# Performance work log

Measured on AMD Instinct MI355X. Metric: run time of the kernel, lower is better.

The kernel has to match this reference:

```python
import jax, jax.numpy as jnp
import numpy as np

N, IN, HID, HEADS, FFN = 2048, 768, 1024, 8, 2048
NH = HID // HEADS  # 128 per-head hidden


def setup_inputs() -> dict:
    key = jax.random.key(0)
    ks = jax.random.split(key, 24)
    s = 0.02
    inp = {
        "feature": jax.random.normal(ks[0], (1, N, IN), jnp.float32),
        "adj": jax.random.bernoulli(ks[1], 0.05, (1, N, N)).astype(jnp.float32),
        "gat1_W1": jax.random.normal(ks[2], (IN, HID), jnp.float32) * s,
        "gat1_a1": jax.random.normal(ks[3], (2 * NH,), jnp.float32) * s,
        "gat1_W2": jax.random.normal(ks[4], (HID, IN), jnp.float32) * s,
        "gat1_a2": jax.random.normal(ks[5], (2 * IN,), jnp.float32) * s,
        "gat2_W1": jax.random.normal(ks[6], (IN, HID), jnp.float32) * s,
        "gat2_a1": jax.random.normal(ks[7], (2 * NH,), jnp.float32) * s,
        "gat2_W2": jax.random.normal(ks[8], (HID, IN), jnp.float32) * s,
        "gat2_a2": jax.random.normal(ks[9], (2 * IN,), jnp.float32) * s,
        "Wf": jax.random.normal(ks[10], (2 * IN, IN), jnp.float32) * s,
        "bf": jnp.zeros((IN,), jnp.float32),
        "ffn_W1": jax.random.normal(ks[11], (IN, FFN), jnp.float32) * s,
        "ffn_b1": jnp.zeros((FFN,), jnp.float32),
        "ffn_W2": jax.random.normal(ks[12], (FFN, FFN), jnp.float32) * s,
        "ffn_b2": jnp.zeros((FFN,), jnp.float32),
        "ffn_W3": jax.random.normal(ks[13], (FFN, IN), jnp.float32) * s,
        "ffn_b3": jnp.zeros((IN,), jnp.float32),
        "out_W1": jax.random.normal(ks[14], (IN, FFN), jnp.float32) * s,
        "out_b1": jnp.zeros((FFN,), jnp.float32),
        "out_W2": jax.random.normal(ks[15], (FFN, IN), jnp.float32) * s,
        "out_b2": jnp.zeros((IN,), jnp.float32),
    }
    return inp


def leaky(x, slope):
    return jnp.where(x >= 0, x, slope * x)


def gat_layer(h, adjb, W, a, heads, concat):
    # h: [N, F_in]; adjb: [N, N] bool. Scores decompose since attn weight is
    # shared across heads: e_ij = leaky(a_l . g_i + a_r . g_j).
    n = h.shape[0]
    g = (h @ W).reshape(n, heads, -1)           # [N, H, F']
    f = g.shape[-1]
    gl = jnp.einsum("nhf,f->nh", g, a[:f])
    gr = jnp.einsum("nhf,f->nh", g, a[f:])
    e = leaky(gl[:, None, :] + gr[None, :, :], 0.2)   # [N, N, H]
    e = jnp.where(adjb[:, :, None], e, jnp.float32(-1e9))
    att = jax.nn.softmax(e, axis=1)             # softmax over source j
    out = jnp.einsum("ijh,jhf->ihf", att, g)    # [N, H, F']
    return out.reshape(n, -1) if concat else out.mean(axis=1)


def gat(x, adj2d, W1, a1, W2, a2):
    adjb = adj2d != 0
    x1 = jax.nn.elu(gat_layer(x, adjb, W1, a1, HEADS, True))
    return gat_layer(x1, adjb, W2, a2, 1, False)


def reference(feature, adj, gat1_W1, gat1_a1, gat1_W2, gat1_a2,
              gat2_W1, gat2_a1, gat2_W2, gat2_a2, Wf, bf,
              ffn_W1, ffn_b1, ffn_W2, ffn_b2, ffn_W3, ffn_b3,
              out_W1, out_b1, out_W2, out_b2):
    sen_adj = adj.at[:, :, -6:].set(0.0)
    sec_adj = jnp.zeros_like(adj).at[:, :, -6:].set(adj[:, :, -6:])
    x = feature[0]                               # [N, IN]
    f_sen = gat(x, sen_adj[0], gat1_W1, gat1_a1, gat1_W2, gat1_a2) + x
    f_sec = gat(x, sec_adj[0], gat2_W1, gat2_a1, gat2_W2, gat2_a2) + x
    f = jnp.concatenate([f_sec, f_sen], axis=-1)
    f = leaky(f @ Wf + bf, 0.01)                 # fusion linear + leaky
    # ffn: MLP(layers=3, keep_last=False) -> act on every layer
    f = leaky(f @ ffn_W1 + ffn_b1, 0.01)
    f = leaky(f @ ffn_W2 + ffn_b2, 0.01)
    f = leaky(f @ ffn_W3 + ffn_b3, 0.01)
    # out_ffn: MLP(layers=2)
    o = leaky(f @ out_W1 + out_b1, 0.01)
    o = leaky(o @ out_W2 + out_b2, 0.01)
    return (o + x)[None]                         # residual, [1, N, IN]
```

## Files before the change

kernel.cpp:

```cpp
#include <hip/hip_runtime.h>
#include <hip/hip_bf16.h>
#include <cmath>

#define NN 2048
#define DIN 768
#define DHID 1024
#define NHEADS 8
#define FPRIME 128
#define DFFN 2048
#define SEN_LIM 2042
#define MAXDEG 256

using short8 = __attribute__((ext_vector_type(8))) short;
using f32x4  = __attribute__((ext_vector_type(4))) float;

#if defined(__has_builtin)
#  if __has_builtin(__builtin_amdgcn_global_load_lds)
#    define HAVE_GLL 1
#  endif
#endif
#ifndef HAVE_GLL
#  define HAVE_GLL 0
#endif

__device__ inline unsigned short f2bf(float f) {
    unsigned u = __float_as_uint(f);
    unsigned r = u + 0x7FFFu + ((u >> 16) & 1u);
    return (unsigned short)(r >> 16);
}
__device__ inline float bf2f(unsigned short h) {
    return __uint_as_float(((unsigned)h) << 16);
}
__device__ inline void store_out(float* p, float v) { *p = v; }
__device__ inline void store_out(unsigned short* p, float v) { *p = f2bf(v); }

#if HAVE_GLL
__device__ inline void gll16(const unsigned short* g, unsigned short* l) {
    __builtin_amdgcn_global_load_lds(
        (const __attribute__((address_space(1))) unsigned int*)g,
        (__attribute__((address_space(3))) unsigned int*)l, 16, 0, 0);
}
#endif

__global__ __launch_bounds__(256) void build_nbrs(
    const float* __restrict__ adj,
    unsigned short* __restrict__ sen_idx, int* __restrict__ sen_cnt,
    unsigned short* __restrict__ sec_idx, int* __restrict__ sec_cnt)
{
    const int i = blockIdx.x;
    __shared__ int c_sen, c_sec;
    if (threadIdx.x == 0) { c_sen = 0; c_sec = 0; }
    __syncthreads();
    for (int j4 = threadIdx.x; j4 < NN / 4; j4 += 256) {
        float4 v = *(const float4*)&adj[(size_t)i * NN + j4 * 4];
        float vs[4] = {v.x, v.y, v.z, v.w};
        #pragma unroll
        for (int q = 0; q < 4; ++q) {
            if (vs[q] != 0.0f) {
                int j = j4 * 4 + q;
                if (j < SEN_LIM) {
                    int p = atomicAdd(&c_sen, 1);
                    if (p < MAXDEG) sen_idx[(size_t)i * MAXDEG + p] = (unsigned short)j;
                } else {
                    int p = atomicAdd(&c_sec, 1);
                    if (p < 8) sec_idx[i * 8 + p] = (unsigned short)j;
                }
            }
        }
    }
    __syncthreads();
    if (threadIdx.x == 0) { sen_cnt[i] = min(c_sen, MAXDEG); sec_cnt[i] = min(c_sec, 8); }
}

struct TPJob { const float* s; unsigned short* d; int K, N, start, trans; };
struct TPJobs { TPJob j[11]; };

__global__ __launch_bounds__(256) void mega_tp(TPJobs jobs, int njobs)
{
    __shared__ float t[32][33];
    const int tile = blockIdx.x;
    int ji = 0;
    for (int k = 1; k < 11; ++k)
        if (k < njobs && tile >= jobs.j[k].start) ji = k;
    const TPJob jb = jobs.j[ji];
    const int lt = tile - jb.start;
    const int ntx = jb.N >> 5;
    const int bn = (lt % ntx) * 32, bk = (lt / ntx) * 32;
    const int tx = threadIdx.x & 31, ty = threadIdx.x >> 5;
    if (jb.trans) {
        #pragma unroll
        for (int r = 0; r < 4; ++r)
            t[ty + r * 8][tx] = jb.s[(size_t)(bk + ty + r * 8) * jb.N + bn + tx];
        __syncthreads();
        #pragma unroll
        for (int r = 0; r < 4; ++r) {
            int n = ty + r * 8;
            jb.d[(size_t)(bn + n) * jb.K + bk + tx] = f2bf(t[tx][n]);
        }
    } else {
        #pragma unroll
        for (int r = 0; r < 4; ++r) {
            size_t e = (size_t)(bk + ty + r * 8) * jb.N + bn + tx;
            jb.d[e] = f2bf(jb.s[e]);
        }
    }
}

template<int BM, int BN, typename OUT_T>
__global__ __launch_bounds__(256) void gemm_mfma(
    const unsigned short* __restrict__ A0, const unsigned short* __restrict__ A1,
    const unsigned short* __restrict__ BT0, const unsigned short* __restrict__ BT1,
    const float* __restrict__ bias, const float* __restrict__ resid,
    OUT_T* __restrict__ C0, OUT_T* __restrict__ C1,
    unsigned short* __restrict__ Cb0, unsigned short* __restrict__ Cb1,
    int M, int N, int K, int act)
{
    constexpr int BK = 64;
    constexpr int WR = BM / 64;
    constexpr int WC = 4 / WR;
    constexpr int NF = BN / (WC * 16);
    constexpr int ACH = BM / 32;
    constexpr int BCH = BN / 32;
    __shared__ unsigned short Asm[BM * BK];
    __shared__ unsigned short Bsm[BN * BK];
    const int z = blockIdx.z;
    const unsigned short* A  = z ? A1  : A0;
    const unsigned short* BT = z ? BT1 : BT0;
    OUT_T* C = z ? C1 : C0;
    unsigned short* Cb = z ? Cb1 : Cb0;
    const int tid = threadIdx.x;
    const int lane = tid & 63, w = tid >> 6;
    const int wr = w / WC, wc = w % WC;
    const int bm = blockIdx.y * BM, bn = blockIdx.x * BN;

    f32x4 acc[4][NF];
    #pragma unroll
    for (int mi = 0; mi < 4; ++mi)
        #pragma unroll
        for (int ni = 0; ni < NF; ++ni)
            acc[mi][ni] = (f32x4){0.f, 0.f, 0.f, 0.f};

    const unsigned short* Abase = A + (size_t)bm * K;
    const unsigned short* Bbase = BT + (size_t)bn * K;

    for (int k0 = 0; k0 < K; k0 += BK) {
        __syncthreads();
        #pragma unroll
        for (int c = 0; c < ACH; ++c) {
            int e = (tid + c * 256) * 8;
            int r = e >> 6, kk = e & 63;
            int kks = kk ^ ((r & 7) << 3);
#if HAVE_GLL
            gll16(&Abase[(size_t)r * K + k0 + kks], &Asm[e]);
#else
            *(short8*)&Asm[e] = *(const short8*)&Abase[(size_t)r * K + k0 + kks];
#endif
        }
        #pragma unroll
        for (int c = 0; c < BCH; ++c) {
            int e = (tid + c * 256) * 8;
            int r = e >> 6, kk = e & 63;
            int kks = kk ^ ((r & 7) << 3);
#if HAVE_GLL
            gll16(&Bbase[(size_t)r * K + k0 + kks], &Bsm[e]);
#else
            *(short8*)&Bsm[e] = *(const short8*)&Bbase[(size_t)r * K + k0 + kks];
#endif
        }
        __syncthreads();
        #pragma unroll
        for (int ks = 0; ks < 2; ++ks) {
            short8 af[4], bfv[NF];
            #pragma unroll
            for (int mi = 0; mi < 4; ++mi) {
                int row = wr * 64 + mi * 16 + (lane & 15);
                int col = (ks * 32 + (lane >> 4) * 8) ^ ((row & 7) << 3);
                af[mi] = *(const short8*)&Asm[row * 64 + col];
            }
            #pragma unroll
            for (int ni = 0; ni < NF; ++ni) {
                int row = wc * (BN / WC) + ni * 16 + (lane & 15);
                int col = (ks * 32 + (lane >> 4) * 8) ^ ((row & 7) << 3);
                bfv[ni] = *(const short8*)&Bsm[row * 64 + col];
            }
            #pragma unroll
            for (int mi = 0; mi < 4; ++mi)
                #pragma unroll
                for (int ni = 0; ni < NF; ++ni)
                    acc[mi][ni] = __builtin_amdgcn_mfma_f32_16x16x32_bf16(
                        af[mi], bfv[ni], acc[mi][ni], 0, 0, 0);
        }
    }

    const int rbase = bm + wr * 64;
    const int cbase = bn + wc * (BN / WC);
    #pragma unroll
    for (int mi = 0; mi < 4; ++mi)
        #pragma unroll
        for (int ni = 0; ni < NF; ++ni)
            #pragma unroll
            for (int r = 0; r < 4; ++r) {
                int grow = rbase + mi * 16 + (lane >> 4) * 4 + r;
                int gcol = cbase + ni * 16 + (lane & 15);
                float v = acc[mi][ni][r];
                if (bias)  v += bias[gcol];
                if (act)   v = (v >= 0.f) ? v : 0.01f * v;
                if (resid) v += resid[(size_t)grow * N + gcol];
                store_out(&C[(size_t)grow * N + gcol], v);
                if (Cb) Cb[(size_t)grow * N + gcol] = f2bf(v);
            }
}

__global__ __launch_bounds__(64) void glgr2(
    const unsigned short* __restrict__ gA, const unsigned short* __restrict__ gB,
    int row_stride, int F, int Hlog2, int nb_per_branch,
    const float* __restrict__ aA, const float* __restrict__ aB,
    float* __restrict__ glA, float* __restrict__ grA,
    float* __restrict__ glB, float* __restrict__ grB,
    float* __restrict__ z, int zblocks)
{
    const int bid = blockIdx.x, lane = threadIdx.x;
    if (bid < zblocks) z[bid * 64 + lane] = 0.f;
    const int br = bid >= nb_per_branch;
    const int b = br ? bid - nb_per_branch : bid;
    const int node = b >> Hlog2, h = b - ((b >> Hlog2) << Hlog2);
    const unsigned short* g = (br ? gB : gA) + (size_t)node * row_stride + h * F;
    const float* a = br ? aB : aA;
    float sl = 0.f, sr = 0.f;
    for (int f = lane; f < F; f += 64) {
        float v = bf2f(g[f]);
        sl += v * a[f];
        sr += v * a[F + f];
    }
    #pragma unroll
    for (int off = 32; off > 0; off >>= 1) {
        sl += __shfl_down(sl, off);
        sr += __shfl_down(sr, off);
    }
    if (lane == 0) {
        (br ? glB : glA)[b] = sl;
        (br ? grB : grA)[b] = sr;
    }
}

__global__ __launch_bounds__(256) void col_mean2(
    const unsigned short* __restrict__ g0, const unsigned short* __restrict__ g1,
    int C, float* __restrict__ o0, float* __restrict__ o1)
{
    const unsigned short* g = blockIdx.z ? g1 : g0;
    float* o = blockIdx.z ? o1 : o0;
    int c = blockIdx.x * 256 + threadIdx.x;
    int r0 = blockIdx.y * 128;
    float s = 0.f;
    for (int r = r0; r < r0 + 128; ++r) s += bf2f(g[(size_t)r * C + c]);
    atomicAdd(&o[c], s * (1.0f / 2048.0f));
}

template<int H, int F, typename OUT_T>
__global__ __launch_bounds__(256) void attn_agg2(
    const unsigned short* __restrict__ gb0, const unsigned short* __restrict__ gb1,
    int g_stride,
    const float* __restrict__ gl0, const float* __restrict__ gr0,
    const float* __restrict__ gl1, const float* __restrict__ gr1,
    const unsigned short* __restrict__ idx0, int is0, const int* __restrict__ cnt0,
    const unsigned short* __restrict__ idx1, int is1, const int* __restrict__ cnt1,
    const float* __restrict__ gmean0, const float* __restrict__ gmean1,
    OUT_T* __restrict__ dst0, OUT_T* __restrict__ dst1,
    int dst_stride, int co0, int co1,
    const float* __restrict__ resid, int mode)
{
    constexpr int HF = H * F;
    const int bid = blockIdx.x;
    const int br = bid >= NN;
    const int i = br ? bid - NN : bid;
    const unsigned short* gbp = br ? gb1 : gb0;
    const float* gl = br ? gl1 : gl0;
    const float* gr = br ? gr1 : gr0;
    const unsigned short* idx = br ? idx1 : idx0;
    const int is = br ? is1 : is0;
    const int* cnt = br ? cnt1 : cnt0;
    const float* gmean = br ? gmean1 : gmean0;
    OUT_T* dst = br ? dst1 : dst0;
    const int co = br ? co1 : co0;

    const int tid = threadIdx.x;
    const int lane = tid & 63, w = tid >> 6;
    const int n = cnt[i];

    if (n == 0) {
        for (int c = tid; c < HF; c += 256) {
            float v = gmean[c];
            if (mode == 0) v = (v > 0.f) ? v : expm1f(v);
            else           v += resid[(size_t)i * HF + c];
            store_out(&dst[(size_t)i * dst_stride + co + c], v);
        }
        return;
    }

    __shared__ float s_wred[4 * H];
    __shared__ float s_max[H], s_inv[H], s_glh[H];
    __shared__ float s_w[128 * H];
    __shared__ unsigned short s_j[128];

    if (tid < H) s_glh[tid] = gl[(size_t)i * H + tid];
    __syncthreads();
    float glh[H];
    #pragma unroll
    for (int h = 0; h < H; ++h) glh[h] = s_glh[h];

    const unsigned short* row_idx = idx + (size_t)i * is;

    float pmax[H];
    #pragma unroll
    for (int h = 0; h < H; ++h) pmax[h] = -1e30f;
    for (int jj = tid; jj < n; jj += 256) {
        int j = row_idx[jj];
        if (H == 8) {
            float4 ga = *(const float4*)&gr[(size_t)j * 8];
            float4 gbv = *(const float4*)&gr[(size_t)j * 8 + 4];
            float sc[8] = {ga.x, ga.y, ga.z, ga.w, gbv.x, gbv.y, gbv.z, gbv.w};
            #pragma unroll
            for (int h = 0; h < H; ++h) {
                float s = glh[h] + sc[h];
                s = (s >= 0.f) ? s : 0.2f * s;
                pmax[h] = fmaxf(pmax[h], s);
            }
        } else {
            float s = glh[0] + gr[j];
            s = (s >= 0.f) ? s : 0.2f * s;
            pmax[0] = fmaxf(pmax[0], s);
        }
    }
    #pragma unroll
    for (int h = 0; h < H; ++h)
        #pragma unroll
        for (int off = 32; off > 0; off >>= 1)
            pmax[h] = fmaxf(pmax[h], __shfl_xor(pmax[h], off));
    if (lane == 0)
        #pragma unroll
        for (int h = 0; h < H; ++h) s_wred[w * H + h] = pmax[h];
    __syncthreads();
    if (tid < H)
        s_max[tid] = fmaxf(fmaxf(s_wred[tid], s_wred[H + tid]),
                           fmaxf(s_wred[2 * H + tid], s_wred[3 * H + tid]));
    __syncthreads();
    float mx[H];
    #pragma unroll
    for (int h = 0; h < H; ++h) mx[h] = s_max[h];

    float psum[H];
    #pragma unroll
    for (int h = 0; h < H; ++h) psum[h] = 0.f;
    for (int jj = tid; jj < n; jj += 256) {
        int j = row_idx[jj];
        if (H == 8) {
            float4 ga = *(const float4*)&gr[(size_t)j * 8];
            float4 gbv = *(const float4*)&gr[(size_t)j * 8 + 4];
            float sc[8] = {ga.x, ga.y, ga.z, ga.w, gbv.x, gbv.y, gbv.z, gbv.w};
            #pragma unroll
            for (int h = 0; h < H; ++h) {
                float s = glh[h] + sc[h];
                s = (s >= 0.f) ? s : 0.2f * s;
                psum[h] += expf(s - mx[h]);
            }
        } else {
            float s = glh[0] + gr[j];
            s = (s >= 0.f) ? s : 0.2f * s;
            psum[0] += expf(s - mx[0]);
        }
    }
    #pragma unroll
    for (int h = 0; h < H; ++h)
        #pragma unroll
        for (int off = 32; off > 0; off >>= 1)
            psum[h] += __shfl_xor(psum[h], off);
    if (lane == 0)
        #pragma unroll
        for (int h = 0; h < H; ++h) s_wred[w * H + h] = psum[h];
    __syncthreads();
    if (tid < H)
        s_inv[tid] = 1.f / (s_wred[tid] + s_wred[H + tid] +
                            s_wred[2 * H + tid] + s_wred[3 * H + tid]);

    const int cb = tid * 4;
    const bool active = (cb < HF);
    const int hh = (H == 8) ? (cb >> 7) : 0;
    float a0 = 0.f, a1 = 0.f, a2 = 0.f, a3 = 0.f;

    for (int c0 = 0; c0 < n; c0 += 128) {
        int m = min(128, n - c0);
        __syncthreads();
        for (int e = tid; e < m * H; e += 256) {
            int jj = (H == 8) ? (e >> 3) : e;
            int h  = (H == 8) ? (e & 7) : 0;
            int j = row_idx[c0 + jj];
            float s = glh[h] + gr[(size_t)j * H + h];
            s = (s >= 0.f) ? s : 0.2f * s;
            s_w[jj * H + h] = expf(s - s_max[h]) * s_inv[h];
            if (h == 0) s_j[jj] = (unsigned short)j;
        }
        __syncthreads();
        if (active) {
            int jj = 0;
            for (; jj + 8 <= m; jj += 8) {
                ushort4 v[8]; float wv[8];
                #pragma unroll
                for (int u = 0; u < 8; ++u) {
                    v[u] = *(const ushort4*)&gbp[(size_t)s_j[jj + u] * g_stride + cb];
                    wv[u] = s_w[(jj + u) * H + hh];
                }
                #pragma unroll
                for (int u = 0; u < 8; ++u) {
                    a0 += wv[u] * bf2f(v[u].x);
                    a1 += wv[u] * bf2f(v[u].y);
                    a2 += wv[u] * bf2f(v[u].z);
                    a3 += wv[u] * bf2f(v[u].w);
                }
            }
            for (; jj < m; ++jj) {
                ushort4 v0 = *(const ushort4*)&gbp[(size_t)s_j[jj] * g_stride + cb];
                float w0 = s_w[jj * H + hh];
                a0 += w0 * bf2f(v0.x); a1 += w0 * bf2f(v0.y);
                a2 += w0 * bf2f(v0.z); a3 += w0 * bf2f(v0.w);
            }
        }
    }

    if (active) {
        float vv[4] = {a0, a1, a2, a3};
        #pragma unroll
        for (int q = 0; q < 4; ++q) {
            float v = vv[q];
            if (mode == 0) v = (v > 0.f) ? v : expm1f(v);
            else           v += resid[(size_t)i * HF + cb + q];
            store_out(&dst[(size_t)i * dst_stride + co + cb + q], v);
        }
    }
}

extern "C" void kernel_launch(void* const* d_in, const int* in_sizes, int n_in,
                              void* d_out, int out_size, void* d_ws, size_t ws_size,
                              hipStream_t stream)
{
    const float* feature = (const float*)d_in[0];
    const float* adj     = (const float*)d_in[1];
    const float* g1W1 = (const float*)d_in[2];
    const float* g1a1 = (const float*)d_in[3];
    const float* g1W2 = (const float*)d_in[4];
    const float* g1a2 = (const float*)d_in[5];
    const float* g2W1 = (const float*)d_in[6];
    const float* g2a1 = (const float*)d_in[7];
    const float* g2W2 = (const float*)d_in[8];
    const float* g2a2 = (const float*)d_in[9];
    const float* Wf  = (const float*)d_in[10];
    const float* bfv = (const float*)d_in[11];
    const float* fW1 = (const float*)d_in[12];
    const float* fb1 = (const float*)d_in[13];
    const float* fW2 = (const float*)d_in[14];
    const float* fb2 = (const float*)d_in[15];
    const float* fW3 = (const float*)d_in[16];
    const float* fb3 = (const float*)d_in[17];
    const float* oW1 = (const float*)d_in[18];
    const float* ob1 = (const float*)d_in[19];
    const float* oW2 = (const float*)d_in[20];
    const float* ob2 = (const float*)d_in[21];
    float* out = (float*)d_out;

    char* ws = (char*)d_ws;
    size_t off = 0;
    auto alloc = [&](size_t bytes) -> void* {
        void* p = ws + off;
        off = (off + bytes + 255) & ~(size_t)255;
        return p;
    };
    typedef unsigned short bf_t;
    int* sen_cnt = (int*)alloc((size_t)NN * 4);
    int* sec_cnt = (int*)alloc((size_t)NN * 4);
    unsigned short* sen_idx = (unsigned short*)alloc((size_t)NN * MAXDEG * 2);
    unsigned short* sec_idx = (unsigned short*)alloc((size_t)NN * 8 * 2);
    bf_t*  g1b   = (bf_t*)alloc((size_t)NN * 2048 * 2);
    float* gl1a  = (float*)alloc((size_t)NN * NHEADS * 4);
    float* gr1a  = (float*)alloc((size_t)NN * NHEADS * 4);
    float* gl1b  = (float*)alloc((size_t)NN * NHEADS * 4);
    float* gr1b  = (float*)alloc((size_t)NN * NHEADS * 4);
    bf_t*  x1a   = (bf_t*)alloc((size_t)NN * DHID * 2);
    bf_t*  x1b   = (bf_t*)alloc((size_t)NN * DHID * 2);
    bf_t*  g2aB  = (bf_t*)alloc((size_t)NN * DIN * 2);
    bf_t*  g2bB  = (bf_t*)alloc((size_t)NN * DIN * 2);
    float* gl2a  = (float*)alloc((size_t)NN * 4);
    float* gr2a  = (float*)alloc((size_t)NN * 4);
    float* gl2b  = (float*)alloc((size_t)NN * 4);
    float* gr2b  = (float*)alloc((size_t)NN * 4);
    float* gmeanL1 = (float*)alloc((size_t)2048 * 4);
    float* gmeanL2 = (float*)alloc((size_t)1536 * 4);
    bf_t*  fcat  = (bf_t*)alloc((size_t)NN * (2 * DIN) * 2);
    bf_t*  fbuf  = (bf_t*)alloc((size_t)NN * DIN * 2);
    bf_t*  tA    = (bf_t*)alloc((size_t)NN * DFFN * 2);
    bf_t*  tB    = (bf_t*)alloc((size_t)NN * DFFN * 2);
    bf_t*  featb = (bf_t*)alloc((size_t)NN * DIN * 2);
    bf_t* W1T_AB = (bf_t*)alloc((size_t)2048 * DIN * 2);
    bf_t* g1W2T = (bf_t*)alloc((size_t)DHID * DIN * 2);
    bf_t* g2W2T = (bf_t*)alloc((size_t)DHID * DIN * 2);
    bf_t* WfT   = (bf_t*)alloc((size_t)(2 * DIN) * DIN * 2);
    bf_t* fW1T  = (bf_t*)alloc((size_t)DIN * DFFN * 2);
    bf_t* fW2T  = (bf_t*)alloc((size_t)DFFN * DFFN * 2);
    bf_t* fW3T  = (bf_t*)alloc((size_t)DFFN * DIN * 2);
    bf_t* oW1T  = (bf_t*)alloc((size_t)DIN * DFFN * 2);
    bf_t* oW2T  = (bf_t*)alloc((size_t)DFFN * DIN * 2);

    build_nbrs<<<NN, 256, 0, stream>>>(adj, sen_idx, sen_cnt, sec_idx, sec_cnt);

    TPJobs jobs;
    int cur = 0, nj = 0;
    auto addjob = [&](const float* s, bf_t* d, int K, int N, int trans) {
        jobs.j[nj] = {s, d, K, N, cur, trans};
        cur += (K / 32) * (N / 32);
        ++nj;
    };
    addjob(g1W1, W1T_AB, DIN, DHID, 1);
    addjob(g2W1, W1T_AB + (size_t)1024 * DIN, DIN, DHID, 1);
    addjob(g1W2, g1W2T, DHID, DIN, 1);
    addjob(g2W2, g2W2T, DHID, DIN, 1);
    addjob(Wf, WfT, 2 * DIN, DIN, 1);
    addjob(fW1, fW1T, DIN, DFFN, 1);
    addjob(fW2, fW2T, DFFN, DFFN, 1);
    addjob(fW3, fW3T, DFFN, DIN, 1);
    addjob(oW1, oW1T, DIN, DFFN, 1);
    addjob(oW2, oW2T, DFFN, DIN, 1);
    addjob(feature, featb, NN, DIN, 0);
    mega_tp<<<cur, 256, 0, stream>>>(jobs, nj);

    gemm_mfma<64, 128, bf_t><<<dim3(2048 / 128, NN / 64, 1), 256, 0, stream>>>(
        featb, nullptr, W1T_AB, nullptr, nullptr, nullptr,
        g1b, nullptr, nullptr, nullptr, NN, 2048, DIN, 0);

    glgr2<<<2 * NN * NHEADS, 64, 0, stream>>>(
        g1b, g1b + 1024, 2048, FPRIME, 3, NN * NHEADS,
        g1a1, g2a1, gl1a, gr1a, gl1b, gr1b, gmeanL1, 32);
    col_mean2<<<dim3(2048 / 256, 16, 1), 256, 0, stream>>>(
        g1b, nullptr, 2048, gmeanL1, nullptr);
    attn_agg2<NHEADS, FPRIME, bf_t><<<2 * NN, 256, 0, stream>>>(
        g1b, g1b + 1024, 2048,
        gl1a, gr1a, gl1b, gr1b,
        sen_idx, MAXDEG, sen_cnt, sec_idx, 8, sec_cnt,
        gmeanL1, gmeanL1 + 1024,
        x1a, x1b, DHID, 0, 0, nullptr, 0);

    gemm_mfma<64, 64, bf_t><<<dim3(DIN / 64, NN / 64, 2), 256, 0, stream>>>(
        x1a, x1b, g1W2T, g2W2T, nullptr, nullptr,
        g2aB, g2bB, nullptr, nullptr, NN, DIN, DHID, 0);

    glgr2<<<2 * NN, 64, 0, stream>>>(
        g2aB, g2bB, DIN, DIN, 0, NN,
        g1a2, g2a2, gl2a, gr2a, gl2b, gr2b, gmeanL2, 24);
    col_mean2<<<dim3(DIN / 256, 16, 2), 256, 0, stream>>>(
        g2aB, g2bB, DIN, gmeanL2, gmeanL2 + DIN);
    attn_agg2<1, DIN, bf_t><<<2 * NN, 256, 0, stream>>>(
        g2aB, g2bB, DIN,
        gl2a, gr2a, gl2b, gr2b,
        sen_idx, MAXDEG, sen_cnt, sec_idx, 8, sec_cnt,
        gmeanL2, gmeanL2 + DIN,
        fcat, fcat, 2 * DIN, DIN, 0, feature, 1);

    gemm_mfma<64, 64, bf_t><<<dim3(DIN / 64, NN / 64, 1), 256, 0, stream>>>(
        fcat, nullptr, WfT, nullptr, bfv, nullptr,
        fbuf, nullptr, nullptr, nullptr, NN, DIN, 2 * DIN, 1);
    gemm_mfma<64, 128, bf_t><<<dim3(DFFN / 128, NN / 64, 1), 256, 0, stream>>>(
        fbuf, nullptr, fW1T, nullptr, fb1, nullptr,
        tA, nullptr, nullptr, nullptr, NN, DFFN, DIN, 1);
    gemm_mfma<64, 128, bf_t><<<dim3(DFFN / 128, NN / 64, 1), 256, 0, stream>>>(
        tA, nullptr, fW2T, nullptr, fb2, nullptr,
        tB, nullptr, nullptr, nullptr, NN, DFFN, DFFN, 1);
    gemm_mfma<64, 64, bf_t><<<dim3(DIN / 64, NN / 64, 1), 256, 0, stream>>>(
        tB, nullptr, fW3T, nullptr, fb3, nullptr,
        fbuf, nullptr, nullptr, nullptr, NN, DIN, DFFN, 1);
    gemm_mfma<64, 128, bf_t><<<dim3(DFFN / 128, NN / 64, 1), 256, 0, stream>>>(
        fbuf, nullptr, oW1T, nullptr, ob1, nullptr,
        tA, nullptr, nullptr, nullptr, NN, DFFN, DIN, 1);
    gemm_mfma<64, 64, float><<<dim3(DIN / 64, NN / 64, 1), 256, 0, stream>>>(
        tA, nullptr, oW2T, nullptr, ob2, feature,
        out, nullptr, nullptr, nullptr, NN, DIN, DFFN, 1);
}
```

Baseline: 447.3 us.

## Double-buffer LDS tiles in bf16 GEMM with vmcnt-based async prefetch

Converts the GEMM main loop to a two-stage LDS pipeline. The next K-tile is issued via global_load_lds into the alternate buffer before computing on the current one, and an explicit s_waitcnt vmcnt plus raw s_barrier stand in for __syncthreads. The aim is to hide global-load latency behind MFMA work. It doubles LDS usage, which may lower occupancy, and it relies on the vmcnt count matching the number of outstanding loads. On the non-GLL fallback path the waitcnt semantics differ, and raw s_barrier does not wait for LDS writes.

```diff
diff --git a/kernel.cpp b/kernel.cpp
--- a/kernel.cpp
+++ b/kernel.cpp
@@ -41,6 +41,13 @@
         (__attribute__((address_space(3))) unsigned int*)l, 16, 0, 0);
 }
 #endif
+
+template<int S> __device__ inline void wait_vmcnt() {
+    if constexpr (S == 0)      asm volatile("s_waitcnt vmcnt(0)" ::: "memory");
+    else if constexpr (S == 4) asm volatile("s_waitcnt vmcnt(4)" ::: "memory");
+    else if constexpr (S == 6) asm volatile("s_waitcnt vmcnt(6)" ::: "memory");
+    else                       asm volatile("s_waitcnt vmcnt(8)" ::: "memory");
+}
 
 __global__ __launch_bounds__(256) void build_nbrs(
     const float* __restrict__ adj,
@@ -121,8 +128,9 @@
     constexpr int NF = BN / (WC * 16);
     constexpr int ACH = BM / 32;
     constexpr int BCH = BN / 32;
-    __shared__ unsigned short Asm[BM * BK];
-    __shared__ unsigned short Bsm[BN * BK];
+    constexpr int S = ACH + BCH;
+    __shared__ unsigned short Asm[2][BM * BK];
+    __shared__ unsigned short Bsm[2][BN * BK];
     const int z = blockIdx.z;
     const unsigned short* A  = z ? A1  : A0;
     const unsigned short* BT = z ? BT1 : BT0;
@@ -143,17 +151,16 @@
     const unsigned short* Abase = A + (size_t)bm * K;
     const unsigned short* Bbase = BT + (size_t)bn * K;
 
-    for (int k0 = 0; k0 < K; k0 += BK) {
-        __syncthreads();
+    auto stage = [&](int b, int k0) {
         #pragma unroll
         for (int c = 0; c < ACH; ++c) {
             int e = (tid + c * 256) * 8;
             int r = e >> 6, kk = e & 63;
             int kks = kk ^ ((r & 7) << 3);
 #if HAVE_GLL
-            gll16(&Abase[(size_t)r * K + k0 + kks], &Asm[e]);
+            gll16(&Abase[(size_t)r * K + k0 + kks], &Asm[b][e]);
 #else
-            *(short8*)&Asm[e] = *(const short8*)&Abase[(size_t)r * K + k0 + kks];
+            *(short8*)&Asm[b][e] = *(const short8*)&Abase[(size_t)r * K + k0 + kks];
 #endif
         }
         #pragma unroll
@@ -162,12 +169,24 @@
             int r = e >> 6, kk = e & 63;
             int kks = kk ^ ((r & 7) << 3);
 #if HAVE_GLL
-            gll16(&Bbase[(size_t)r * K + k0 + kks], &Bsm[e]);
+            gll16(&Bbase[(size_t)r * K + k0 + kks], &Bsm[b][e]);
 #else
-            *(short8*)&Bsm[e] = *(const short8*)&Bbase[(size_t)r * K + k0 + kks];
+            *(short8*)&Bsm[b][e] = *(const short8*)&Bbase[(size_t)r * K + k0 + kks];
 #endif
         }
-        __syncthreads();
+    };
+
+    const int nk = K / BK;
+    stage(0, 0);
+    int buf = 0;
+    for (int t = 0; t < nk; ++t) {
+        if (t + 1 < nk) {
+            stage(buf ^ 1, (t + 1) * BK);
+            wait_vmcnt<S>();
+        } else {
+            wait_vmcnt<0>();
+        }
+        __builtin_amdgcn_s_barrier();
         #pragma unroll
         for (int ks = 0; ks < 2; ++ks) {
             short8 af[4], bfv[NF];
@@ -175,13 +194,13 @@
             for (int mi = 0; mi < 4; ++mi) {
                 int row = wr * 64 + mi * 16 + (lane & 15);
                 int col = (ks * 32 + (lane >> 4) * 8) ^ ((row & 7) << 3);
-                af[mi] = *(const short8*)&Asm[row * 64 + col];
+                af[mi] = *(const short8*)&Asm[buf][row * 64 + col];
             }
             #pragma unroll
             for (int ni = 0; ni < NF; ++ni) {
                 int row = wc * (BN / WC) + ni * 16 + (lane & 15);
                 int col = (ks * 32 + (lane >> 4) * 8) ^ ((row & 7) << 3);
-                bfv[ni] = *(const short8*)&Bsm[row * 64 + col];
+                bfv[ni] = *(const short8*)&Bsm[buf][row * 64 + col];
             }
             #pragma unroll
             for (int mi = 0; mi < 4; ++mi)
@@ -190,6 +209,8 @@
                     acc[mi][ni] = __builtin_amdgcn_mfma_f32_16x16x32_bf16(
                         af[mi], bfv[ni], acc[mi][ni], 0, 0, 0);
         }
+        __builtin_amdgcn_s_barrier();
+        buf ^= 1;
     }
 
     const int rbase = bm + wr * 64;
```

Result: no change. 441.6 us (-1.3%).
